# Kernel optimization log

Hardware: AMD Instinct MI355X
Metric: run time of the kernel (lower is better)

The kernel has to match this reference:

```python
import jax, jax.numpy as jnp
import numpy as np

CLASS_PERIOD = 360  # window width per object class


def setup_inputs() -> dict:
    key = jax.random.key(0)
    k1, k2, k3 = jax.random.split(key, 3)
    B, C, P = 16384, 12, CLASS_PERIOD
    preds = jax.random.normal(k1, (B, C * P), dtype=jnp.float32)
    labels = jax.random.uniform(k2, (B, C * P), dtype=jnp.float32)
    obj_classes = jax.random.randint(k3, (B,), 0, C, dtype=jnp.int64)
    return {"preds": preds, "labels": labels, "obj_classes": obj_classes}


def reference(preds, labels, obj_classes):
    P = CLASS_PERIOD
    # gather per-sample window of width P starting at obj_class * P
    idx = obj_classes[:, None] * P + jnp.arange(P)[None, :]  # [B, P]
    pw = jnp.take_along_axis(preds, idx, axis=1)             # [B, P]
    lw = jnp.take_along_axis(labels, idx, axis=1)            # [B, P]
    # scale by L1 norm of the window, then log-softmax over the window
    scaled = pw / jnp.sum(jnp.abs(pw), axis=1, keepdims=True)
    ls = jax.nn.log_softmax(scaled, axis=1)
    # mean=False branch: per-instance sum, accumulated (negated) over batch
    loss = -jnp.sum(lw * ls)
    return loss.reshape(1)
```

## Files before the change

### kernel.cpp

```cpp
#include <hip/hip_runtime.h>
#include <math.h>

#define CLASS_P 360
#define ROW_STRIDE 4320
#define NF4 90
#define RPW 4

__device__ __forceinline__ float wave_sum(float v) {
    #pragma unroll
    for (int o = 32; o > 0; o >>= 1) v += __shfl_xor(v, o);
    return v;
}
__device__ __forceinline__ float wave_max(float v) {
    #pragma unroll
    for (int o = 32; o > 0; o >>= 1) v = fmaxf(v, __shfl_xor(v, o));
    return v;
}

__global__ __launch_bounds__(256) void vp_rows(
        const float* __restrict__ preds,
        const float* __restrict__ labels,
        const int*   __restrict__ cls,
        float* __restrict__ partial,
        int B) {
    const int wid  = threadIdx.x >> 6;
    const int lane = threadIdx.x & 63;
    const int wave = blockIdx.x * 4 + wid;
    const int r0   = wave * RPW;
    const bool has2 = lane < (NF4 - 64);

    float4 a0[RPW], b0[RPW], a1[RPW], b1[RPW];
    float  wgt[RPW];

    #pragma unroll
    for (int k = 0; k < RPW; k++) {
        const int r  = r0 + k;
        const int rr = (r < B) ? r : 0;
        wgt[k] = (r < B) ? 1.0f : 0.0f;
        const size_t base = (size_t)rr * ROW_STRIDE + (size_t)cls[rr] * CLASS_P;
        const float4* __restrict__ p4 = (const float4*)(preds + base);
        const float4* __restrict__ l4 = (const float4*)(labels + base);
        a0[k] = p4[lane];
        b0[k] = l4[lane];
        a1[k] = make_float4(0.f, 0.f, 0.f, 0.f);
        b1[k] = a1[k];
        if (has2) { a1[k] = p4[lane + 64]; b1[k] = l4[lane + 64]; }
    }

    float acc = 0.f;
    #pragma unroll
    for (int k = 0; k < RPW; k++) {
        float sabs = fabsf(a0[k].x) + fabsf(a0[k].y) + fabsf(a0[k].z) + fabsf(a0[k].w)
                   + fabsf(a1[k].x) + fabsf(a1[k].y) + fabsf(a1[k].z) + fabsf(a1[k].w);
        float pmax = fmaxf(fmaxf(a0[k].x, a0[k].y), fmaxf(a0[k].z, a0[k].w));
        if (has2)
            pmax = fmaxf(pmax, fmaxf(fmaxf(a1[k].x, a1[k].y), fmaxf(a1[k].z, a1[k].w)));
        sabs = wave_sum(sabs);
        pmax = wave_max(pmax);

        const float inv = 1.0f / sabs;
        const float m   = pmax * inv;

        float se = __expf(a0[k].x * inv - m) + __expf(a0[k].y * inv - m)
                 + __expf(a0[k].z * inv - m) + __expf(a0[k].w * inv - m);
        if (has2)
            se += __expf(a1[k].x * inv - m) + __expf(a1[k].y * inv - m)
                + __expf(a1[k].z * inv - m) + __expf(a1[k].w * inv - m);
        se = wave_sum(se);
        const float lse = __logf(se) + m;

        float t = b0[k].x * (lse - a0[k].x * inv) + b0[k].y * (lse - a0[k].y * inv)
                + b0[k].z * (lse - a0[k].z * inv) + b0[k].w * (lse - a0[k].w * inv);
        if (has2)
            t += b1[k].x * (lse - a1[k].x * inv) + b1[k].y * (lse - a1[k].y * inv)
               + b1[k].z * (lse - a1[k].z * inv) + b1[k].w * (lse - a1[k].w * inv);
        acc += wgt[k] * t;
    }
    acc = wave_sum(acc);

    __shared__ float sm[4];
    if (lane == 0) sm[wid] = acc;
    __syncthreads();
    if (threadIdx.x == 0) partial[blockIdx.x] = sm[0] + sm[1] + sm[2] + sm[3];
}

__global__ __launch_bounds__(256) void vp_reduce(
        const float* __restrict__ partial, float* __restrict__ out, int n) {
    __shared__ float sm[4];
    float acc = 0.f;
    for (int i = threadIdx.x; i < n; i += 256) acc += partial[i];
    acc = wave_sum(acc);
    const int wid = threadIdx.x >> 6, lane = threadIdx.x & 63;
    if (lane == 0) sm[wid] = acc;
    __syncthreads();
    if (threadIdx.x == 0) out[0] = sm[0] + sm[1] + sm[2] + sm[3];
}

extern "C" void kernel_launch(void* const* d_in, const int* in_sizes, int n_in,
                              void* d_out, int out_size, void* d_ws, size_t ws_size,
                              hipStream_t stream) {
    const float* preds  = (const float*)d_in[0];
    const float* labels = (const float*)d_in[1];
    const int*   cls    = (const int*)d_in[2];
    float* out = (float*)d_out;
    float* ws  = (float*)d_ws;

    const int B = in_sizes[2];
    const int rows_per_block = 4 * RPW;
    const int blocks = (B + rows_per_block - 1) / rows_per_block;

    vp_rows<<<blocks, 256, 0, stream>>>(preds, labels, cls, ws, B);
    vp_reduce<<<1, 256, 0, stream>>>(ws, out, blocks);
}
```

Baseline: 19.66 us.

## Fold log-softmax loss algebraically, batch wave reductions, replace reduce kernel with atomics

The per-row loss is rewritten as lse*sum(l) - inv*sum(l*p). The label sums and the label-times-pred dot product are then reduced in the same shuffle pass as the L1 norm. The max subtraction is dropped, since the scaled values lie in [-1,1], which removes one full wave reduction per row. Rows per wave drop from 4 to 2. The second reduction kernel is replaced by a memset plus one atomicAdd per block, which adds atomic contention on a single address and makes float summation order nondeterministic.

After: 42.13 us. +114.3%, slower.

```diff
diff --git a/kernel.cpp b/kernel.cpp
--- a/kernel.cpp
+++ b/kernel.cpp
@@ -4,96 +4,84 @@
 #define CLASS_P 360
 #define ROW_STRIDE 4320
 #define NF4 90
-#define RPW 4
+#define RPW 2
+#define WPB 4
 
-__device__ __forceinline__ float wave_sum(float v) {
-    #pragma unroll
-    for (int o = 32; o > 0; o >>= 1) v += __shfl_xor(v, o);
-    return v;
-}
-__device__ __forceinline__ float wave_max(float v) {
-    #pragma unroll
-    for (int o = 32; o > 0; o >>= 1) v = fmaxf(v, __shfl_xor(v, o));
-    return v;
-}
-
-__global__ __launch_bounds__(256) void vp_rows(
+__global__ __launch_bounds__(256) void vp_main(
         const float* __restrict__ preds,
         const float* __restrict__ labels,
         const int*   __restrict__ cls,
-        float* __restrict__ partial,
+        float* __restrict__ out,
         int B) {
     const int wid  = threadIdx.x >> 6;
     const int lane = threadIdx.x & 63;
-    const int wave = blockIdx.x * 4 + wid;
-    const int r0   = wave * RPW;
+    const int r0   = (blockIdx.x * WPB + wid) * RPW;
     const bool has2 = lane < (NF4 - 64);
 
-    float4 a0[RPW], b0[RPW], a1[RPW], b1[RPW];
-    float  wgt[RPW];
+    float4 a0[RPW], a1[RPW];
+    float sabs[RPW], sl[RPW], slp[RPW], wgt[RPW];
 
     #pragma unroll
-    for (int k = 0; k < RPW; k++) {
+    for (int k = 0; k < RPW; ++k) {
         const int r  = r0 + k;
         const int rr = (r < B) ? r : 0;
         wgt[k] = (r < B) ? 1.0f : 0.0f;
         const size_t base = (size_t)rr * ROW_STRIDE + (size_t)cls[rr] * CLASS_P;
         const float4* __restrict__ p4 = (const float4*)(preds + base);
         const float4* __restrict__ l4 = (const float4*)(labels + base);
+
         a0[k] = p4[lane];
-        b0[k] = l4[lane];
+        float4 b0 = l4[lane];
         a1[k] = make_float4(0.f, 0.f, 0.f, 0.f);
-        b1[k] = a1[k];
-        if (has2) { a1[k] = p4[lane + 64]; b1[k] = l4[lane + 64]; }
+        float4 b1 = make_float4(0.f, 0.f, 0.f, 0.f);
+        if (has2) { a1[k] = p4[lane + 64]; b1 = l4[lane + 64]; }
+
+        sabs[k] = fabsf(a0[k].x) + fabsf(a0[k].y) + fabsf(a0[k].z) + fabsf(a0[k].w)
+                + fabsf(a1[k].x) + fabsf(a1[k].y) + fabsf(a1[k].z) + fabsf(a1[k].w);
+        sl[k]   = (b0.x + b0.y) + (b0.z + b0.w) + (b1.x + b1.y) + (b1.z + b1.w);
+        slp[k]  = b0.x * a0[k].x + b0.y * a0[k].y + b0.z * a0[k].z + b0.w * a0[k].w
+                + b1.x * a1[k].x + b1.y * a1[k].y + b1.z * a1[k].z + b1.w * a1[k].w;
+    }
+
+    #pragma unroll
+    for (int o = 32; o > 0; o >>= 1) {
+        #pragma unroll
+        for (int k = 0; k < RPW; ++k) {
+            sabs[k] += __shfl_xor(sabs[k], o);
+            sl[k]   += __shfl_xor(sl[k],   o);
+            slp[k]  += __shfl_xor(slp[k],  o);
+        }
+    }
+
+    float inv[RPW], se[RPW];
+    #pragma unroll
+    for (int k = 0; k < RPW; ++k) {
+        inv[k] = 1.0f / sabs[k];
+        float e = __expf(a0[k].x * inv[k]) + __expf(a0[k].y * inv[k])
+                + __expf(a0[k].z * inv[k]) + __expf(a0[k].w * inv[k]);
+        if (has2)
+            e += __expf(a1[k].x * inv[k]) + __expf(a1[k].y * inv[k])
+               + __expf(a1[k].z * inv[k]) + __expf(a1[k].w * inv[k]);
+        se[k] = e;
+    }
+    #pragma unroll
+    for (int o = 32; o > 0; o >>= 1) {
+        #pragma unroll
+        for (int k = 0; k < RPW; ++k) se[k] += __shfl_xor(se[k], o);
     }
 
     float acc = 0.f;
     #pragma unroll
-    for (int k = 0; k < RPW; k++) {
-        float sabs = fabsf(a0[k].x) + fabsf(a0[k].y) + fabsf(a0[k].z) + fabsf(a0[k].w)
-                   + fabsf(a1[k].x) + fabsf(a1[k].y) + fabsf(a1[k].z) + fabsf(a1[k].w);
-        float pmax = fmaxf(fmaxf(a0[k].x, a0[k].y), fmaxf(a0[k].z, a0[k].w));
-        if (has2)
-            pmax = fmaxf(pmax, fmaxf(fmaxf(a1[k].x, a1[k].y), fmaxf(a1[k].z, a1[k].w)));
-        sabs = wave_sum(sabs);
-        pmax = wave_max(pmax);
+    for (int k = 0; k < RPW; ++k) {
+        const float lse = __logf(se[k]);
+        acc += wgt[k] * (lse * sl[k] - inv[k] * slp[k]);
+    }
 
-        const float inv = 1.0f / sabs;
-        const float m   = pmax * inv;
-
-        float se = __expf(a0[k].x * inv - m) + __expf(a0[k].y * inv - m)
-                 + __expf(a0[k].z * inv - m) + __expf(a0[k].w * inv - m);
-        if (has2)
-            se += __expf(a1[k].x * inv - m) + __expf(a1[k].y * inv - m)
-                + __expf(a1[k].z * inv - m) + __expf(a1[k].w * inv - m);
-        se = wave_sum(se);
-        const float lse = __logf(se) + m;
-
-        float t = b0[k].x * (lse - a0[k].x * inv) + b0[k].y * (lse - a0[k].y * inv)
-                + b0[k].z * (lse - a0[k].z * inv) + b0[k].w * (lse - a0[k].w * inv);
-        if (has2)
-            t += b1[k].x * (lse - a1[k].x * inv) + b1[k].y * (lse - a1[k].y * inv)
-               + b1[k].z * (lse - a1[k].z * inv) + b1[k].w * (lse - a1[k].w * inv);
-        acc += wgt[k] * t;
-    }
-    acc = wave_sum(acc);
-
-    __shared__ float sm[4];
+    __shared__ float sm[WPB];
     if (lane == 0) sm[wid] = acc;
     __syncthreads();
-    if (threadIdx.x == 0) partial[blockIdx.x] = sm[0] + sm[1] + sm[2] + sm[3];
-}
-
-__global__ __launch_bounds__(256) void vp_reduce(
-        const float* __restrict__ partial, float* __restrict__ out, int n) {
-    __shared__ float sm[4];
-    float acc = 0.f;
-    for (int i = threadIdx.x; i < n; i += 256) acc += partial[i];
-    acc = wave_sum(acc);
-    const int wid = threadIdx.x >> 6, lane = threadIdx.x & 63;
-    if (lane == 0) sm[wid] = acc;
-    __syncthreads();
-    if (threadIdx.x == 0) out[0] = sm[0] + sm[1] + sm[2] + sm[3];
+    if (threadIdx.x == 0)
+        atomicAdd(out, (sm[0] + sm[1]) + (sm[2] + sm[3]));
 }
 
 extern "C" void kernel_launch(void* const* d_in, const int* in_sizes, int n_in,
@@ -103,12 +91,11 @@
     const float* labels = (const float*)d_in[1];
     const int*   cls    = (const int*)d_in[2];
     float* out = (float*)d_out;
-    float* ws  = (float*)d_ws;
 
     const int B = in_sizes[2];
-    const int rows_per_block = 4 * RPW;
+    const int rows_per_block = WPB * RPW;
     const int blocks = (B + rows_per_block - 1) / rows_per_block;
 
-    vp_rows<<<blocks, 256, 0, stream>>>(preds, labels, cls, ws, B);
-    vp_reduce<<<1, 256, 0, stream>>>(ws, out, blocks);
+    hipMemsetAsync(out, 0, sizeof(float), stream);
+    vp_main<<<blocks, 256, 0, stream>>>(preds, labels, cls, out, B);
 }
```
